# Kernel optimization log

Measured on AMD Instinct MI355X. Metric: run time of the kernel, lower is better.

Reference implementation:

```python
import jax, jax.numpy as jnp
import numpy as np

B, N1, N2, C = 4, 1024, 128, 1152
H, D = 16, 72            # num_heads, head_dim (1152 = 16*72)
HID = 4608               # mlp hidden = 4*1152
ATTN_SCALE = D ** -0.5
RMS_SCALE = C ** 0.5     # quirk: RMSNorm built with dim=1152 though applied over d=72
LN_EPS = 1e-6


def setup_inputs() -> dict:
    key = jax.random.key(0)
    ks = iter(jax.random.split(key, 64))
    n = lambda shape, s=1.0: jax.random.normal(next(ks), shape, jnp.float32) * s
    W = 0.02  # weight init scale
    inp = {
        "x": n((B, N1, C)),
        "c": n((B, N2, C)),
        "global_c": n((B, C)),
        "ada_x_w": n((C, 6 * C), W), "ada_x_b": jnp.zeros((6 * C,)),
        "ada_c_w": n((C, 6 * C), W), "ada_c_b": jnp.zeros((6 * C,)),
        "g1x_g": jnp.ones((C,)), "g1x_b": jnp.zeros((C,)),
        "g2x_g": jnp.ones((C,)), "g2x_b": jnp.zeros((C,)),
        "g1c_g": jnp.ones((C,)), "g1c_b": jnp.zeros((C,)),
        "g2c_g": jnp.ones((C,)), "g2c_b": jnp.zeros((C,)),
        "qkv_x_w": n((C, 3 * C), W), "qkv_x_b": jnp.zeros((3 * C,)),
        "proj_x_w": n((C, C), W), "proj_x_b": jnp.zeros((C,)),
        "qkv_c_w": n((C, 3 * C), W), "qkv_c_b": jnp.zeros((3 * C,)),
        "proj_c_w": n((C, C), W), "proj_c_b": jnp.zeros((C,)),
        "gq_x": jnp.ones((1,)), "gk_x": jnp.ones((1,)),
        "gq_c": jnp.ones((1,)), "gk_c": jnp.ones((1,)),
        "mlp_x_w1": n((C, HID), W), "mlp_x_b1": jnp.zeros((HID,)),
        "mlp_x_w2": n((HID, C), W), "mlp_x_b2": jnp.zeros((C,)),
        "mlp_c_w1": n((C, HID), W), "mlp_c_b1": jnp.zeros((HID,)),
        "mlp_c_w2": n((HID, C), W), "mlp_c_b2": jnp.zeros((C,)),
    }
    return inp


def _ln(t, g, b):
    m = t.mean(-1, keepdims=True)
    v = ((t - m) ** 2).mean(-1, keepdims=True)
    return (t - m) * jax.lax.rsqrt(v + LN_EPS) * g + b


def _modulate(t, shift, scale):  # shift/scale: [B, C]
    return t * (1.0 + scale[:, None, :]) + shift[:, None, :]


def _rms(t, g):  # F.normalize over last dim, then * sqrt(1152) * g
    nrm = jnp.sqrt(jnp.sum(t * t, axis=-1, keepdims=True))
    return t / jnp.maximum(nrm, 1e-12) * (RMS_SCALE * g)


def _heads(t):  # [B, N, H*D] -> [B, H, N, D]
    Bq, Nq, _ = t.shape
    return t.reshape(Bq, Nq, H, D).transpose(0, 2, 1, 3)


def _mmdit_forward(x, c, global_c,
                   ada_x_w, ada_x_b, ada_c_w, ada_c_b,
                   g1x_g, g1x_b, g2x_g, g2x_b, g1c_g, g1c_b, g2c_g, g2c_b,
                   qkv_x_w, qkv_x_b, proj_x_w, proj_x_b,
                   qkv_c_w, qkv_c_b, proj_c_w, proj_c_b,
                   gq_x, gk_x, gq_c, gk_c,
                   mlp_x_w1, mlp_x_b1, mlp_x_w2, mlp_x_b2,
                   mlp_c_w1, mlp_c_b1, mlp_c_w2, mlp_c_b2):
    s = jax.nn.silu(global_c)
    mod_x = jnp.split(s @ ada_x_w + ada_x_b, 6, axis=-1)
    mod_c = jnp.split(s @ ada_c_w + ada_c_b, 6, axis=-1)
    (sh_msa_x, sc_msa_x, gt_msa_x, sh_mlp_x, sc_mlp_x, gt_mlp_x) = mod_x
    (sh_msa_c, sc_msa_c, gt_msa_c, sh_mlp_c, sc_mlp_c, gt_mlp_c) = mod_c

    xin = _modulate(_ln(x, g1x_g, g1x_b), sh_msa_x, sc_msa_x)
    cin = _modulate(_ln(c, g1c_g, g1c_b), sh_msa_c, sc_msa_c)

    qx, kx, vx = jnp.split(xin @ qkv_x_w + qkv_x_b, 3, axis=-1)
    qc, kc, vc = jnp.split(cin @ qkv_c_w + qkv_c_b, 3, axis=-1)
    qx, kx, vx = _heads(qx), _heads(kx), _heads(vx)
    qc, kc, vc = _heads(qc), _heads(kc), _heads(vc)
    qx, kx = _rms(qx, gq_x), _rms(kx, gk_x)
    qc, kc = _rms(qc, gq_c), _rms(kc, gk_c)

    q = jnp.concatenate([qx, qc], axis=2)  # [B,H,N1+N2,D]
    k = jnp.concatenate([kx, kc], axis=2)
    v = jnp.concatenate([vx, vc], axis=2)

    scores = jnp.einsum('bhnd,bhmd->bhnm', q, k) * ATTN_SCALE
    attn = jax.nn.softmax(scores, axis=-1)
    o = jnp.einsum('bhnm,bhmd->bhnd', attn, v)
    o = o.transpose(0, 2, 1, 3).reshape(B, N1 + N2, C)
    ox, oc = o[:, :N1], o[:, N1:]
    attn_x = ox @ proj_x_w + proj_x_b
    attn_c = oc @ proj_c_w + proj_c_b

    x = x + gt_msa_x[:, None, :] * attn_x
    c = c + gt_msa_c[:, None, :] * attn_c

    hx = _modulate(_ln(x, g2x_g, g2x_b), sh_mlp_x, sc_mlp_x)
    hx = jax.nn.gelu(hx @ mlp_x_w1 + mlp_x_b1, approximate=True) @ mlp_x_w2 + mlp_x_b2
    x = x + gt_mlp_x[:, None, :] * hx

    hc = _modulate(_ln(c, g2c_g, g2c_b), sh_mlp_c, sc_mlp_c)
    hc = jax.nn.gelu(hc @ mlp_c_w1 + mlp_c_b1, approximate=True) @ mlp_c_w2 + mlp_c_b2
    c = c + gt_mlp_c[:, None, :] * hc
    return x, c


def reference(x, c, global_c,
              ada_x_w, ada_x_b, ada_c_w, ada_c_b,
              g1x_g, g1x_b, g2x_g, g2x_b, g1c_g, g1c_b, g2c_g, g2c_b,
              qkv_x_w, qkv_x_b, proj_x_w, proj_x_b,
              qkv_c_w, qkv_c_b, proj_c_w, proj_c_b,
              gq_x, gk_x, gq_c, gk_c,
              mlp_x_w1, mlp_x_b1, mlp_x_w2, mlp_x_b2,
              mlp_c_w1, mlp_c_b1, mlp_c_w2, mlp_c_b2):
    return _mmdit_forward(x, c, global_c,
                          ada_x_w, ada_x_b, ada_c_w, ada_c_b,
                          g1x_g, g1x_b, g2x_g, g2x_b, g1c_g, g1c_b, g2c_g, g2c_b,
                          qkv_x_w, qkv_x_b, proj_x_w, proj_x_b,
                          qkv_c_w, qkv_c_b, proj_c_w, proj_c_b,
                          gq_x, gk_x, gq_c, gk_c,
                          mlp_x_w1, mlp_x_b1, mlp_x_w2, mlp_x_b2,
                          mlp_c_w1, mlp_c_b1, mlp_c_w2, mlp_c_b2)
```

## Files before the change

### kernel.cpp

```cpp
#include <hip/hip_runtime.h>

typedef unsigned short u16;
typedef unsigned int u32;
typedef __attribute__((ext_vector_type(8))) short bf16x8;
typedef __attribute__((ext_vector_type(4))) float f32x4;

#define MX_ 4096
#define NT_ 1152
#define C_  1152
#define DP_ 96
#define D_  72
#define H_  16
#define MT_ 4608

static __device__ __forceinline__ float b2f(u16 u){ union{u32 i; float f;} x; x.i=((u32)u)<<16; return x.f; }
static __device__ __forceinline__ u16 f2b(float f){ u32 i=__float_as_uint(f); return (u16)((i + 0x7FFFu + ((i>>16)&1u))>>16); }

static __device__ __forceinline__ void gl_lds16(const u16* g, u16* l){
  __builtin_amdgcn_global_load_lds((const __attribute__((address_space(1))) void*)g,
                                   (__attribute__((address_space(3))) void*)l, 16, 0, 0);
}

#define MFMA16(a,b,c) __builtin_amdgcn_mfma_f32_16x16x32_bf16(a,b,c,0,0,0)

struct TrArgs {
  const float* src[8]; u16* dst[8]; int K[8]; int N[8]; int start[9];
};

__global__ __launch_bounds__(256) void transpose_kernel(TrArgs a){
  int bx = blockIdx.x;
  int mi = 0;
  #pragma unroll
  for (int i = 0; i < 8; ++i) if (bx >= a.start[i+1]) mi = i+1;
  int t = bx - a.start[mi];
  int K = a.K[mi], N = a.N[mi];
  int ntk = K >> 5;
  int tk = t % ntk, tn = t / ntk;
  int k0 = tk*32, n0 = tn*32;
  __shared__ u16 lds[32][33];
  int c = threadIdx.x & 31, r = threadIdx.x >> 5;
  const float* src = a.src[mi];
  u16* dst = a.dst[mi];
  #pragma unroll
  for (int ii = 0; ii < 4; ++ii){
    int row = r + ii*8;
    lds[row][c] = f2b(src[(size_t)(k0+row)*N + n0 + c]);
  }
  __syncthreads();
  #pragma unroll
  for (int ii = 0; ii < 4; ++ii){
    int row = r + ii*8;
    dst[(size_t)(n0+row)*K + k0 + c] = lds[c][row];
  }
}

__global__ __launch_bounds__(256) void ada_kernel(const float* gc, const float* wx, const float* bx,
                                                  const float* wc, const float* bc,
                                                  float* mod_x, float* mod_c){
  __shared__ float s[4][C_];
  __shared__ float part[4][4][64];
  int tid = threadIdx.x;
  for (int i = tid; i < 4*C_; i += 256){
    float v = gc[i];
    s[i / C_][i % C_] = v / (1.f + __expf(-v));
  }
  __syncthreads();
  int jq = tid & 63;
  int kq = tid >> 6;
  int jg = blockIdx.x*64 + jq;
  int which = jg / 6912;
  int j = jg % 6912;
  const float* W = which ? wc : wx;
  float a0=0.f, a1=0.f, a2=0.f, a3=0.f;
  for (int k = kq*288; k < kq*288 + 288; ++k){
    float w = W[(size_t)k*6912 + j];
    a0 += s[0][k]*w; a1 += s[1][k]*w; a2 += s[2][k]*w; a3 += s[3][k]*w;
  }
  part[kq][0][jq]=a0; part[kq][1][jq]=a1; part[kq][2][jq]=a2; part[kq][3][jq]=a3;
  __syncthreads();
  if (kq == 0){
    float bb = (which ? bc : bx)[j];
    float* out = which ? mod_c : mod_x;
    #pragma unroll
    for (int b = 0; b < 4; ++b){
      out[(size_t)b*6912 + j] = part[0][b][jq] + part[1][b][jq] + part[2][b][jq] + part[3][b][jq] + bb;
    }
  }
}

__global__ __launch_bounds__(256) void ln_mod_kernel(
  const float* srcx, const float* srcc, const float* g, const float* bt,
  const float* gcn, const float* btc,
  const float* shx, const float* scx, const float* shc, const float* scc,
  u16* out)
{
  int m = blockIdx.x;
  bool isC = (m >= MX_);
  const float* src = isC ? srcc + (size_t)(m - MX_)*C_ : srcx + (size_t)m*C_;
  int bidx = isC ? ((m - MX_) >> 7) : (m >> 10);
  const float* gg = isC ? gcn : g;
  const float* bb = isC ? btc : bt;
  const float* sh = (isC ? shc : shx) + (size_t)bidx*6912;
  const float* sc = (isC ? scc : scx) + (size_t)bidx*6912;
  int tid = threadIdx.x;
  float lv[8];
  float sum = 0.f, sq = 0.f;
  if (tid < 144){
    float4 v0 = *(const float4*)(src + tid*8);
    float4 v1 = *(const float4*)(src + tid*8 + 4);
    lv[0]=v0.x; lv[1]=v0.y; lv[2]=v0.z; lv[3]=v0.w;
    lv[4]=v1.x; lv[5]=v1.y; lv[6]=v1.z; lv[7]=v1.w;
    #pragma unroll
    for (int j = 0; j < 8; ++j){ sum += lv[j]; sq += lv[j]*lv[j]; }
  }
  #pragma unroll
  for (int off = 1; off < 64; off <<= 1){ sum += __shfl_xor(sum, off); sq += __shfl_xor(sq, off); }
  __shared__ float rs[4], rq[4];
  int wave = tid >> 6, lane = tid & 63;
  if (lane == 0){ rs[wave] = sum; rq[wave] = sq; }
  __syncthreads();
  float S = rs[0]+rs[1]+rs[2]+rs[3];
  float Q = rq[0]+rq[1]+rq[2]+rq[3];
  float mean = S * (1.f/1152.f);
  float var  = Q * (1.f/1152.f) - mean*mean;
  float rstd = rsqrtf(var + 1e-6f);
  if (tid < 144){
    union { uint4 v; u16 s[8]; } o;
    #pragma unroll
    for (int j = 0; j < 8; ++j){
      int n = tid*8 + j;
      float val = (lv[j] - mean)*rstd*gg[n] + bb[n];
      val = val*(1.f + sc[n]) + sh[n];
      o.s[j] = f2b(val);
    }
    *(uint4*)(out + (size_t)m*C_ + tid*8) = o.v;
  }
}

__global__ __launch_bounds__(256) void reduce2_kernel(
  const float* p,
  const float* residx, const float* residc,
  const float* modx, const float* modc,
  const float* biasx, const float* biasc,
  float* outx, float* outc)
{
  for (int i4 = blockIdx.x*256 + threadIdx.x; i4 < MT_*288; i4 += gridDim.x*256){
    int m = i4 / 288, n4 = (i4 % 288)*4;
    bool isC = (m >= MX_);
    int bidx = isC ? ((m - MX_) >> 7) : (m >> 10);
    const float* gate  = (isC ? modc : modx) + (size_t)bidx*6912;
    const float* bias  = isC ? biasc : biasx;
    const float* resid = isC ? residc + (size_t)(m - MX_)*C_ : residx + (size_t)m*C_;
    float* o = isC ? outc + (size_t)(m - MX_)*C_ : outx + (size_t)m*C_;
    float4 a = *(const float4*)(p + (size_t)m*C_ + n4);
    float4 b = *(const float4*)(p + (size_t)(MT_ + m)*C_ + n4);
    float4 r = *(const float4*)(resid + n4);
    float4 ov;
    ov.x = r.x + gate[n4+0]*(a.x + b.x + bias[n4+0]);
    ov.y = r.y + gate[n4+1]*(a.y + b.y + bias[n4+1]);
    ov.z = r.z + gate[n4+2]*(a.z + b.z + bias[n4+2]);
    ov.w = r.w + gate[n4+3]*(a.w + b.w + bias[n4+3]);
    *(float4*)(o + n4) = ov;
  }
}

struct GemmArgs {
  const u16* A; int lda; int rowmap;
  const u16* BTx; const u16* BTc;
  const float* biasx; const float* biasc;
  void* outx; void* outc;
  const float* residx; const float* residc;
  const float* gatex; const float* gatec;
  int N, K, kLen;
};

static __device__ __forceinline__ int amap(int m, int rowmap){
  if (rowmap){
    if (m < MX_) return (m >> 10)*NT_ + (m & 1023);
    int mm = m - MX_;
    return (mm >> 7)*NT_ + 1024 + (mm & 127);
  }
  return m;
}

template<int EPI>
__global__ __launch_bounds__(256, 2) void gemm_kernel(GemmArgs g){
  __shared__ u16 As[128*64];
  __shared__ u16 Bs[128*64];
  int gx = gridDim.x, gy = gridDim.y;
  int nwg = gx*gy;
  int orig = blockIdx.y*gx + blockIdx.x;
  int q = nwg >> 3, r8 = nwg & 7;
  int xcd = orig & 7, wi = orig >> 3;
  int swz = (xcd < r8 ? xcd*(q+1) : r8*(q+1) + (xcd - r8)*q) + wi;
  int n0 = (swz % gx)*128, m0 = (swz / gx)*128;
  int kStart = blockIdx.z * g.kLen;
  bool isC = (m0 >= MX_);
  const u16* BT = isC ? g.BTc : g.BTx;
  int tid = threadIdx.x, wave = tid >> 6, lane = tid & 63;
  int lg = lane >> 4, lr = lane & 15;
  int wm = wave >> 1, wn = wave & 1;
  f32x4 acc[4][4] = {};

  const u16* Aaddr[4]; const u16* Baddr[4];
  #pragma unroll
  for (int i = 0; i < 4; ++i){
    int cb = (wave*4 + i)*64;
    int qq = cb + lane;
    int row = qq >> 3;
    int c16 = (qq & 7) ^ (row & 7);
    Aaddr[i] = g.A + (size_t)amap(m0 + row, g.rowmap)*g.lda + kStart + c16*8;
    Baddr[i] = BT + (size_t)(n0 + row)*g.K + kStart + c16*8;
  }
  for (int k0 = 0; k0 < g.kLen; k0 += 64){
    #pragma unroll
    for (int i = 0; i < 4; ++i){
      int cb = (wave*4 + i)*64;
      gl_lds16(Aaddr[i] + k0, As + cb*8);
      gl_lds16(Baddr[i] + k0, Bs + cb*8);
    }
    __syncthreads();
    #pragma unroll
    for (int kkI = 0; kkI < 2; ++kkI){
      bf16x8 af[4], bfr[4];
      #pragma unroll
      for (int mi = 0; mi < 4; ++mi){
        int row = wm*64 + mi*16 + lr;
        int c16 = (kkI*4 + lg) ^ (row & 7);
        af[mi] = *(const bf16x8*)&As[row*64 + c16*8];
      }
      #pragma unroll
      for (int ni = 0; ni < 4; ++ni){
        int row = wn*64 + ni*16 + lr;
        int c16 = (kkI*4 + lg) ^ (row & 7);
        bfr[ni] = *(const bf16x8*)&Bs[row*64 + c16*8];
      }
      #pragma unroll
      for (int mi = 0; mi < 4; ++mi)
        #pragma unroll
        for (int ni = 0; ni < 4; ++ni)
          acc[mi][ni] = MFMA16(af[mi], bfr[ni], acc[mi][ni]);
    }
    __syncthreads();
  }

  const float* bias  = isC ? g.biasc : g.biasx;
  const float* resid = isC ? g.residc : g.residx;
  void* out = isC ? g.outc : g.outx;
  const float* gate = nullptr;
  if (EPI == 2){
    int bidx = isC ? ((m0 - MX_) >> 7) : (m0 >> 10);
    gate = (isC ? g.gatec : g.gatex) + (size_t)bidx*6912;
  }
  int mbase = isC ? (m0 - MX_) : m0;
  float* pbase = nullptr;
  if (EPI == 3) pbase = (float*)g.outx + (size_t)blockIdx.z*MT_*C_;
  #pragma unroll
  for (int mi = 0; mi < 4; ++mi){
    #pragma unroll
    for (int r = 0; r < 4; ++r){
      #pragma unroll
      for (int ni = 0; ni < 4; ++ni){
        int n = n0 + wn*64 + ni*16 + lr;
        if (EPI == 3){
          size_t prow = (size_t)(m0 + wm*64 + mi*16 + lg*4 + r);
          pbase[prow*(size_t)g.N + n] = acc[mi][ni][r];
        } else {
          size_t orow = (size_t)(mbase + wm*64 + mi*16 + lg*4 + r);
          float v = acc[mi][ni][r] + bias[n];
          if (EPI == 1){
            float u = 0.7978845608028654f*(v + 0.044715f*v*v*v);
            v = 0.5f*v*(1.f + tanhf(u));
          }
          if (EPI == 2){
            v = resid[orow*(size_t)g.N + n] + gate[n]*v;
            ((float*)out)[orow*(size_t)g.N + n] = v;
          } else {
            ((u16*)out)[orow*(size_t)g.N + n] = f2b(v);
          }
        }
      }
    }
  }
}

__global__ __launch_bounds__(256) void rmshead_kernel(
  const u16* qkv, const float* gqx, const float* gkx, const float* gqc, const float* gkc,
  u16* qpad, u16* kpad, u16* vT)
{
  int tt = blockIdx.x, h = blockIdx.y, b = blockIdx.z;
  int t0 = tt*64;
  bool isC = (t0 >= 1024);
  size_t rowbase = isC ? (size_t)(MX_ + b*128 + (t0 - 1024)) : (size_t)(b*1024 + t0);
  __shared__ u16 sq[2][64][72];
  __shared__ u16 sv[64][72];
  __shared__ float nf[2][64];
  int tid = threadIdx.x;
  for (int s = tid; s < 1728; s += 256){
    int which = s / 576, rem = s % 576;
    int t = rem / 9, ch = rem % 9;
    uint4 v = *(const uint4*)(qkv + (rowbase + t)*3456 + which*C_ + h*D_ + ch*8);
    u16* dst = (which < 2) ? &sq[which][t][ch*8] : &sv[t][ch*8];
    *(uint4*)dst = v;
  }
  __syncthreads();
  {
    int row = tid >> 1, half = tid & 1;
    int which = row >> 6, t = row & 63;
    float ss = 0.f;
    for (int d = half*36; d < half*36 + 36; ++d){
      float v = b2f(sq[which][t][d]); ss += v*v;
    }
    ss += __shfl_xor(ss, 1);
    if (half == 0){
      const float* gp = (which == 0) ? (isC ? gqc : gqx) : (isC ? gkc : gkx);
      float f = 33.9411254970f * gp[0] / fmaxf(sqrtf(ss), 1e-12f);
      if (which == 0) f *= 0.11785113019775793f;
      nf[which][t] = f;
    }
  }
  __syncthreads();
  size_t obase = ((size_t)(b*H_ + h)*NT_ + t0) * DP_;
  for (int s = tid; s < 1536; s += 256){
    int which = s / 768, rem = s % 768;
    int t = rem / 12, ch = rem % 12;
    float f = nf[which][t];
    union { uint4 v; u16 e[8]; } o;
    #pragma unroll
    for (int j = 0; j < 8; ++j){
      int d = ch*8 + j;
      o.e[j] = (d < D_) ? f2b(b2f(sq[which][t][d]) * f) : (u16)0;
    }
    *(uint4*)((which == 0 ? qpad : kpad) + obase + (size_t)t*DP_ + ch*8) = o.v;
  }
  size_t vbase = (size_t)(b*H_ + h)*80*NT_;
  for (int s = tid; s < 576; s += 256){
    int d = s / 8, ch = s % 8;
    union { uint4 v; u16 e[8]; } o;
    #pragma unroll
    for (int j = 0; j < 8; ++j) o.e[j] = sv[ch*8 + j][d];
    *(uint4*)(vT + vbase + (size_t)d*NT_ + t0 + ch*8) = o.v;
  }
  for (int s = tid; s < 512; s += 256){
    int d = 72 + (s >> 6), t = s & 63;
    vT[vbase + (size_t)d*NT_ + t0 + t] = (d == 72) ? (u16)0x3F80 : (u16)0;
  }
}

__global__ __launch_bounds__(256) void attn_kernel(
  const u16* qpad, const u16* kpad, const u16* vT, u16* O)
{
  __shared__ u16 Ps[4][32][40];
  int qtb = blockIdx.x, h = blockIdx.y, b = blockIdx.z;
  int bh = b*H_ + h;
  int tid = threadIdx.x, wave = tid >> 6, lane = tid & 63;
  int lg = lane >> 4, lr = lane & 15;
  int q0 = qtb*128 + wave*32;

  const u16* qb = qpad + (size_t)bh*NT_*DP_;
  const u16* kb = kpad + (size_t)bh*NT_*DP_;
  const u16* vb = vT + (size_t)bh*80*NT_;

  bf16x8 qf[2][3];
  #pragma unroll
  for (int qt = 0; qt < 2; ++qt)
    #pragma unroll
    for (int kk = 0; kk < 3; ++kk)
      qf[qt][kk] = *(const bf16x8*)(qb + (size_t)(q0 + qt*16 + lr)*DP_ + kk*32 + lg*8);

  f32x4 acc[5][2] = {};
  float m0 = -1e30f, m1 = -1e30f;

  bf16x8 kfA[2][3], kfB[2][3], vf[5];
  auto LOADK = [&](bf16x8 (&kf)[2][3], int kvt){
    #pragma unroll
    for (int kt = 0; kt < 2; ++kt)
      #pragma unroll
      for (int kk = 0; kk < 3; ++kk)
        kf[kt][kk] = *(const bf16x8*)(kb + (size_t)(kvt*32 + kt*16 + lr)*DP_ + kk*32 + lg*8);
  };
  u16* prow0 = &Ps[wave][lr][0];
  u16* prow1 = &Ps[wave][16 + lr][0];

  auto TILE = [&](bf16x8 (&kf)[2][3], bf16x8 (&kfn)[2][3], int t){
    #pragma unroll
    for (int dc = 0; dc < 5; ++dc)
      vf[dc] = *(const bf16x8*)(vb + (size_t)(dc*16 + lr)*NT_ + t*32 + lg*8);
    if (t + 1 < 36) LOADK(kfn, t + 1);

    f32x4 st[2][2] = {};
    __builtin_amdgcn_s_setprio(1);
    #pragma unroll
    for (int kk = 0; kk < 3; ++kk){
      st[0][0] = MFMA16(kf[0][kk], qf[0][kk], st[0][0]);
      st[0][1] = MFMA16(kf[0][kk], qf[1][kk], st[0][1]);
      st[1][0] = MFMA16(kf[1][kk], qf[0][kk], st[1][0]);
      st[1][1] = MFMA16(kf[1][kk], qf[1][kk], st[1][1]);
    }
    __builtin_amdgcn_s_setprio(0);

    float pm0 = fmaxf(fmaxf(fmaxf(st[0][0][0], st[0][0][1]), fmaxf(st[0][0][2], st[0][0][3])),
                      fmaxf(fmaxf(st[1][0][0], st[1][0][1]), fmaxf(st[1][0][2], st[1][0][3])));
    float pm1 = fmaxf(fmaxf(fmaxf(st[0][1][0], st[0][1][1]), fmaxf(st[0][1][2], st[0][1][3])),
                      fmaxf(fmaxf(st[1][1][0], st[1][1][1]), fmaxf(st[1][1][2], st[1][1][3])));
    float tt = fmaxf(pm0 - m0, pm1 - m1);
    if (!__all(tt <= 8.f)){
      float r0 = fmaxf(pm0, __shfl_xor(pm0, 16)); r0 = fmaxf(r0, __shfl_xor(r0, 32));
      float r1 = fmaxf(pm1, __shfl_xor(pm1, 16)); r1 = fmaxf(r1, __shfl_xor(r1, 32));
      float n0 = fmaxf(m0, r0), n1 = fmaxf(m1, r1);
      float f0 = __expf(m0 - n0), f1 = __expf(m1 - n1);
      m0 = n0; m1 = n1;
      #pragma unroll
      for (int dc = 0; dc < 5; ++dc)
        #pragma unroll
        for (int j = 0; j < 4; ++j){ acc[dc][0][j] *= f0; acc[dc][1][j] *= f1; }
    }
    #pragma unroll
    for (int kt = 0; kt < 2; ++kt){
      #pragma unroll
      for (int qt = 0; qt < 2; ++qt){
        float mm = qt ? m1 : m0;
        u32 w0 = (u32)f2b(__expf(st[kt][qt][0] - mm)) | ((u32)f2b(__expf(st[kt][qt][1] - mm)) << 16);
        u32 w1 = (u32)f2b(__expf(st[kt][qt][2] - mm)) | ((u32)f2b(__expf(st[kt][qt][3] - mm)) << 16);
        uint2 pkd; pkd.x = w0; pkd.y = w1;
        *(uint2*)((qt ? prow1 : prow0) + kt*16 + lg*4) = pkd;
      }
    }
    asm volatile("s_waitcnt lgkmcnt(0)" ::: "memory");
    __builtin_amdgcn_sched_barrier(0);
    bf16x8 bp0 = *(const bf16x8*)(prow0 + lg*8);
    bf16x8 bp1 = *(const bf16x8*)(prow1 + lg*8);
    __builtin_amdgcn_s_setprio(1);
    #pragma unroll
    for (int dc = 0; dc < 5; ++dc){
      acc[dc][0] = MFMA16(vf[dc], bp0, acc[dc][0]);
      acc[dc][1] = MFMA16(vf[dc], bp1, acc[dc][1]);
    }
    __builtin_amdgcn_s_setprio(0);
  };

  LOADK(kfA, 0);
  for (int t2 = 0; t2 < 18; ++t2){
    TILE(kfA, kfB, 2*t2);
    TILE(kfB, kfA, 2*t2 + 1);
  }

  float l0 = __shfl(acc[4][0][0], 32 + lr);
  float l1 = __shfl(acc[4][1][0], 32 + lr);
  float rl0 = 1.f / l0, rl1 = 1.f / l1;
  #pragma unroll
  for (int dc = 0; dc < 5; ++dc){
    #pragma unroll
    for (int qt = 0; qt < 2; ++qt){
      if (dc < 4 || lg < 2){
        float rl = qt ? rl1 : rl0;
        union { uint2 v; u16 e[4]; } o;
        #pragma unroll
        for (int j = 0; j < 4; ++j) o.e[j] = f2b(acc[dc][qt][j] * rl);
        int tok = q0 + qt*16 + lr;
        *(uint2*)(O + ((size_t)b*NT_ + tok)*C_ + h*D_ + dc*16 + lg*4) = o.v;
      }
    }
  }
}

extern "C" void kernel_launch(void* const* d_in, const int* in_sizes, int n_in,
                              void* d_out, int out_size, void* d_ws, size_t ws_size,
                              hipStream_t stream)
{
  (void)in_sizes; (void)n_in; (void)out_size; (void)ws_size;
  const float* x        = (const float*)d_in[0];
  const float* c        = (const float*)d_in[1];
  const float* gc       = (const float*)d_in[2];
  const float* ada_x_w  = (const float*)d_in[3];
  const float* ada_x_b  = (const float*)d_in[4];
  const float* ada_c_w  = (const float*)d_in[5];
  const float* ada_c_b  = (const float*)d_in[6];
  const float* g1x_g    = (const float*)d_in[7];
  const float* g1x_b    = (const float*)d_in[8];
  const float* g2x_g    = (const float*)d_in[9];
  const float* g2x_b    = (const float*)d_in[10];
  const float* g1c_g    = (const float*)d_in[11];
  const float* g1c_b    = (const float*)d_in[12];
  const float* g2c_g    = (const float*)d_in[13];
  const float* g2c_b    = (const float*)d_in[14];
  const float* qkv_x_w  = (const float*)d_in[15];
  const float* qkv_x_b  = (const float*)d_in[16];
  const float* proj_x_w = (const float*)d_in[17];
  const float* proj_x_b = (const float*)d_in[18];
  const float* qkv_c_w  = (const float*)d_in[19];
  const float* qkv_c_b  = (const float*)d_in[20];
  const float* proj_c_w = (const float*)d_in[21];
  const float* proj_c_b = (const float*)d_in[22];
  const float* gq_x     = (const float*)d_in[23];
  const float* gk_x     = (const float*)d_in[24];
  const float* gq_c     = (const float*)d_in[25];
  const float* gk_c     = (const float*)d_in[26];
  const float* m_x_w1   = (const float*)d_in[27];
  const float* m_x_b1   = (const float*)d_in[28];
  const float* m_x_w2   = (const float*)d_in[29];
  const float* m_x_b2   = (const float*)d_in[30];
  const float* m_c_w1   = (const float*)d_in[31];
  const float* m_c_b1   = (const float*)d_in[32];
  const float* m_c_w2   = (const float*)d_in[33];
  const float* m_c_b2   = (const float*)d_in[34];
  float* out = (float*)d_out;

  char* ws = (char*)d_ws;
  size_t off = 0;
  auto alloc = [&](size_t bytes)->void*{ void* p = ws + off; off += (bytes + 255) & ~(size_t)255; return p; };
  u16* WTqx  = (u16*)alloc((size_t)3456*1152*2);
  u16* WTqc  = (u16*)alloc((size_t)3456*1152*2);
  u16* WTpx  = (u16*)alloc((size_t)1152*1152*2);
  u16* WTpc  = (u16*)alloc((size_t)1152*1152*2);
  u16* WTm1x = (u16*)alloc((size_t)4608*1152*2);
  u16* WTm2x = (u16*)alloc((size_t)1152*4608*2);
  u16* WTm1c = (u16*)alloc((size_t)4608*1152*2);
  u16* WTm2c = (u16*)alloc((size_t)1152*4608*2);
  float* mod_x = (float*)alloc((size_t)4*6912*4);
  float* mod_c = (float*)alloc((size_t)4*6912*4);
  u16* xin  = (u16*)alloc((size_t)4608*1152*2);
  u16* pool = (u16*)alloc((size_t)4608*4608*2);
  u16* qpad = (u16*)alloc((size_t)64*1152*96*2 + 4096);
  u16* kpad = (u16*)alloc((size_t)64*1152*96*2 + 4096);
  u16* vTb  = (u16*)alloc((size_t)64*80*1152*2 + 4096);
  u16* Obuf = (u16*)alloc((size_t)4*1152*1152*2);
  float* x1c1 = (float*)alloc((size_t)4608*1152*4);
  float* fc2p = (float*)qpad;

  {
    TrArgs ta;
    const float* srcs[8] = {qkv_x_w, qkv_c_w, proj_x_w, proj_c_w, m_x_w1, m_x_w2, m_c_w1, m_c_w2};
    u16* dsts[8]         = {WTqx, WTqc, WTpx, WTpc, WTm1x, WTm2x, WTm1c, WTm2c};
    int Ks[8] = {1152,1152,1152,1152,1152,4608,1152,4608};
    int Ns[8] = {3456,3456,1152,1152,4608,1152,4608,1152};
    int st = 0;
    for (int i = 0; i < 8; ++i){
      ta.src[i] = srcs[i]; ta.dst[i] = dsts[i]; ta.K[i] = Ks[i]; ta.N[i] = Ns[i];
      ta.start[i] = st; st += (Ks[i]/32)*(Ns[i]/32);
    }
    ta.start[8] = st;
    transpose_kernel<<<dim3(st), dim3(256), 0, stream>>>(ta);
  }
  ada_kernel<<<dim3(216), dim3(256), 0, stream>>>(gc, ada_x_w, ada_x_b, ada_c_w, ada_c_b, mod_x, mod_c);
  ln_mod_kernel<<<dim3(4608), dim3(256), 0, stream>>>(
      x, c, g1x_g, g1x_b, g1c_g, g1c_b,
      mod_x + 0, mod_x + 1152, mod_c + 0, mod_c + 1152, xin);
  {
    GemmArgs ga{};
    ga.A = xin; ga.lda = 1152; ga.rowmap = 0;
    ga.BTx = WTqx; ga.BTc = WTqc; ga.biasx = qkv_x_b; ga.biasc = qkv_c_b;
    ga.outx = pool; ga.outc = pool + (size_t)4096*3456;
    ga.N = 3456; ga.K = 1152; ga.kLen = 1152;
    gemm_kernel<0><<<dim3(27,36), dim3(256), 0, stream>>>(ga);
  }
  rmshead_kernel<<<dim3(18,16,4), dim3(256), 0, stream>>>(pool, gq_x, gk_x, gq_c, gk_c, qpad, kpad, vTb);
  attn_kernel<<<dim3(9,16,4), dim3(256), 0, stream>>>(qpad, kpad, vTb, Obuf);
  {
    GemmArgs ga{};
    ga.A = Obuf; ga.lda = 1152; ga.rowmap = 1;
    ga.BTx = WTpx; ga.BTc = WTpc; ga.biasx = proj_x_b; ga.biasc = proj_c_b;
    ga.outx = x1c1; ga.outc = x1c1 + (size_t)4096*1152;
    ga.residx = x; ga.residc = c;
    ga.gatex = mod_x + 2*1152; ga.gatec = mod_c + 2*1152;
    ga.N = 1152; ga.K = 1152; ga.kLen = 1152;
    gemm_kernel<2><<<dim3(9,36), dim3(256), 0, stream>>>(ga);
  }
  ln_mod_kernel<<<dim3(4608), dim3(256), 0, stream>>>(
      x1c1, x1c1 + (size_t)4096*1152, g2x_g, g2x_b, g2c_g, g2c_b,
      mod_x + 3*1152, mod_x + 4*1152, mod_c + 3*1152, mod_c + 4*1152, xin);
  {
    GemmArgs ga{};
    ga.A = xin; ga.lda = 1152; ga.rowmap = 0;
    ga.BTx = WTm1x; ga.BTc = WTm1c; ga.biasx = m_x_b1; ga.biasc = m_c_b1;
    ga.outx = pool; ga.outc = pool + (size_t)4096*4608;
    ga.N = 4608; ga.K = 1152; ga.kLen = 1152;
    gemm_kernel<1><<<dim3(36,36), dim3(256), 0, stream>>>(ga);
  }
  {
    GemmArgs ga{};
    ga.A = pool; ga.lda = 4608; ga.rowmap = 0;
    ga.BTx = WTm2x; ga.BTc = WTm2c;
    ga.outx = fc2p;
    ga.N = 1152; ga.K = 4608; ga.kLen = 2304;
    gemm_kernel<3><<<dim3(9,36,2), dim3(256), 0, stream>>>(ga);
  }
  reduce2_kernel<<<dim3(2048), dim3(256), 0, stream>>>(
      fc2p, x1c1, x1c1 + (size_t)4096*1152,
      mod_x + 5*1152, mod_c + 5*1152, m_x_b2, m_c_b2,
      out, out + (size_t)4096*1152);
}
```

Measured before the change: 454.9 us.

## Halve attention query tile per wave and remap blocks across XCDs

The attention kernel now gives each wave 16 query rows instead of 32, so each block covers 64 queries and the grid grows from 576 to 1152 blocks. The launch becomes a 1D grid whose block index is remapped so consecutive dispatches land on the same (batch, head), which is meant to improve K/V cache locality per XCD. Launch bounds request 4 blocks per CU to raise occupancy. The cost is that each K/V tile is loaded and reused for half as many queries, which doubles K/V traffic and lowers MFMA work per load.

```diff
diff --git a/kernel.cpp b/kernel.cpp
--- a/kernel.cpp
+++ b/kernel.cpp
@@ -347,29 +347,30 @@
   }
 }
 
-__global__ __launch_bounds__(256) void attn_kernel(
+__global__ __launch_bounds__(256, 4) void attn_kernel(
   const u16* qpad, const u16* kpad, const u16* vT, u16* O)
 {
-  __shared__ u16 Ps[4][32][40];
-  int qtb = blockIdx.x, h = blockIdx.y, b = blockIdx.z;
+  __shared__ u16 Ps[4][16][40];
+  int orig = blockIdx.x;
+  int w = (orig & 7)*144 + (orig >> 3);
+  int qtb = w % 18, hb = w / 18;
+  int h = hb & 15, b = hb >> 4;
   int bh = b*H_ + h;
   int tid = threadIdx.x, wave = tid >> 6, lane = tid & 63;
   int lg = lane >> 4, lr = lane & 15;
-  int q0 = qtb*128 + wave*32;
+  int q0 = qtb*64 + wave*16;
 
   const u16* qb = qpad + (size_t)bh*NT_*DP_;
   const u16* kb = kpad + (size_t)bh*NT_*DP_;
   const u16* vb = vT + (size_t)bh*80*NT_;
 
-  bf16x8 qf[2][3];
-  #pragma unroll
-  for (int qt = 0; qt < 2; ++qt)
-    #pragma unroll
-    for (int kk = 0; kk < 3; ++kk)
-      qf[qt][kk] = *(const bf16x8*)(qb + (size_t)(q0 + qt*16 + lr)*DP_ + kk*32 + lg*8);
-
-  f32x4 acc[5][2] = {};
-  float m0 = -1e30f, m1 = -1e30f;
+  bf16x8 qf[3];
+  #pragma unroll
+  for (int kk = 0; kk < 3; ++kk)
+    qf[kk] = *(const bf16x8*)(qb + (size_t)(q0 + lr)*DP_ + kk*32 + lg*8);
+
+  f32x4 acc[5] = {};
+  float m0 = -1e30f;
 
   bf16x8 kfA[2][3], kfB[2][3], vf[5];
   auto LOADK = [&](bf16x8 (&kf)[2][3], int kvt){
@@ -379,8 +380,7 @@
       for (int kk = 0; kk < 3; ++kk)
         kf[kt][kk] = *(const bf16x8*)(kb + (size_t)(kvt*32 + kt*16 + lr)*DP_ + kk*32 + lg*8);
   };
-  u16* prow0 = &Ps[wave][lr][0];
-  u16* prow1 = &Ps[wave][16 + lr][0];
+  u16* prow = &Ps[wave][lr][0];
 
   auto TILE = [&](bf16x8 (&kf)[2][3], bf16x8 (&kfn)[2][3], int t){
     #pragma unroll
@@ -388,54 +388,41 @@
       vf[dc] = *(const bf16x8*)(vb + (size_t)(dc*16 + lr)*NT_ + t*32 + lg*8);
     if (t + 1 < 36) LOADK(kfn, t + 1);
 
-    f32x4 st[2][2] = {};
+    f32x4 st[2] = {};
     __builtin_amdgcn_s_setprio(1);
     #pragma unroll
     for (int kk = 0; kk < 3; ++kk){
-      st[0][0] = MFMA16(kf[0][kk], qf[0][kk], st[0][0]);
-      st[0][1] = MFMA16(kf[0][kk], qf[1][kk], st[0][1]);
-      st[1][0] = MFMA16(kf[1][kk], qf[0][kk], st[1][0]);
-      st[1][1] = MFMA16(kf[1][kk], qf[1][kk], st[1][1]);
+      st[0] = MFMA16(kf[0][kk], qf[kk], st[0]);
+      st[1] = MFMA16(kf[1][kk], qf[kk], st[1]);
     }
     __builtin_amdgcn_s_setprio(0);
 
-    float pm0 = fmaxf(fmaxf(fmaxf(st[0][0][0], st[0][0][1]), fmaxf(st[0][0][2], st[0][0][3])),
-                      fmaxf(fmaxf(st[1][0][0], st[1][0][1]), fmaxf(st[1][0][2], st[1][0][3])));
-    float pm1 = fmaxf(fmaxf(fmaxf(st[0][1][0], st[0][1][1]), fmaxf(st[0][1][2], st[0][1][3])),
-                      fmaxf(fmaxf(st[1][1][0], st[1][1][1]), fmaxf(st[1][1][2], st[1][1][3])));
-    float tt = fmaxf(pm0 - m0, pm1 - m1);
-    if (!__all(tt <= 8.f)){
+    float pm0 = fmaxf(fmaxf(fmaxf(st[0][0], st[0][1]), fmaxf(st[0][2], st[0][3])),
+                      fmaxf(fmaxf(st[1][0], st[1][1]), fmaxf(st[1][2], st[1][3])));
+    if (!__all(pm0 - m0 <= 8.f)){
       float r0 = fmaxf(pm0, __shfl_xor(pm0, 16)); r0 = fmaxf(r0, __shfl_xor(r0, 32));
-      float r1 = fmaxf(pm1, __shfl_xor(pm1, 16)); r1 = fmaxf(r1, __shfl_xor(r1, 32));
-      float n0 = fmaxf(m0, r0), n1 = fmaxf(m1, r1);
-      float f0 = __expf(m0 - n0), f1 = __expf(m1 - n1);
-      m0 = n0; m1 = n1;
+      float n0 = fmaxf(m0, r0);
+      float f0 = __expf(m0 - n0);
+      m0 = n0;
       #pragma unroll
       for (int dc = 0; dc < 5; ++dc)
         #pragma unroll
-        for (int j = 0; j < 4; ++j){ acc[dc][0][j] *= f0; acc[dc][1][j] *= f1; }
+        for (int j = 0; j < 4; ++j) acc[dc][j] *= f0;
     }
     #pragma unroll
     for (int kt = 0; kt < 2; ++kt){
-      #pragma unroll
-      for (int qt = 0; qt < 2; ++qt){
-        float mm = qt ? m1 : m0;
-        u32 w0 = (u32)f2b(__expf(st[kt][qt][0] - mm)) | ((u32)f2b(__expf(st[kt][qt][1] - mm)) << 16);
-        u32 w1 = (u32)f2b(__expf(st[kt][qt][2] - mm)) | ((u32)f2b(__expf(st[kt][qt][3] - mm)) << 16);
-        uint2 pkd; pkd.x = w0; pkd.y = w1;
-        *(uint2*)((qt ? prow1 : prow0) + kt*16 + lg*4) = pkd;
-      }
+      u32 w0 = (u32)f2b(__expf(st[kt][0] - m0)) | ((u32)f2b(__expf(st[kt][1] - m0)) << 16);
+      u32 w1 = (u32)f2b(__expf(st[kt][2] - m0)) | ((u32)f2b(__expf(st[kt][3] - m0)) << 16);
+      uint2 pkd; pkd.x = w0; pkd.y = w1;
+      *(uint2*)(prow + kt*16 + lg*4) = pkd;
     }
     asm volatile("s_waitcnt lgkmcnt(0)" ::: "memory");
     __builtin_amdgcn_sched_barrier(0);
-    bf16x8 bp0 = *(const bf16x8*)(prow0 + lg*8);
-    bf16x8 bp1 = *(const bf16x8*)(prow1 + lg*8);
+    bf16x8 bp = *(const bf16x8*)(prow + lg*8);
     __builtin_amdgcn_s_setprio(1);
     #pragma unroll
-    for (int dc = 0; dc < 5; ++dc){
-      acc[dc][0] = MFMA16(vf[dc], bp0, acc[dc][0]);
-      acc[dc][1] = MFMA16(vf[dc], bp1, acc[dc][1]);
-    }
+    for (int dc = 0; dc < 5; ++dc)
+      acc[dc] = MFMA16(vf[dc], bp, acc[dc]);
     __builtin_amdgcn_s_setprio(0);
   };
 
@@ -445,21 +432,16 @@
     TILE(kfB, kfA, 2*t2 + 1);
   }
 
-  float l0 = __shfl(acc[4][0][0], 32 + lr);
-  float l1 = __shfl(acc[4][1][0], 32 + lr);
-  float rl0 = 1.f / l0, rl1 = 1.f / l1;
+  float l0 = __shfl(acc[4][0], 32 + lr);
+  float rl0 = 1.f / l0;
   #pragma unroll
   for (int dc = 0; dc < 5; ++dc){
-    #pragma unroll
-    for (int qt = 0; qt < 2; ++qt){
-      if (dc < 4 || lg < 2){
-        float rl = qt ? rl1 : rl0;
-        union { uint2 v; u16 e[4]; } o;
-        #pragma unroll
-        for (int j = 0; j < 4; ++j) o.e[j] = f2b(acc[dc][qt][j] * rl);
-        int tok = q0 + qt*16 + lr;
-        *(uint2*)(O + ((size_t)b*NT_ + tok)*C_ + h*D_ + dc*16 + lg*4) = o.v;
-      }
+    if (dc < 4 || lg < 2){
+      union { uint2 v; u16 e[4]; } o;
+      #pragma unroll
+      for (int j = 0; j < 4; ++j) o.e[j] = f2b(acc[dc][j] * rl0);
+      int tok = q0 + lr;
+      *(uint2*)(O + ((size_t)b*NT_ + tok)*C_ + h*D_ + dc*16 + lg*4) = o.v;
     }
   }
 }
@@ -555,7 +537,7 @@
     gemm_kernel<0><<<dim3(27,36), dim3(256), 0, stream>>>(ga);
   }
   rmshead_kernel<<<dim3(18,16,4), dim3(256), 0, stream>>>(pool, gq_x, gk_x, gq_c, gk_c, qpad, kpad, vTb);
-  attn_kernel<<<dim3(9,16,4), dim3(256), 0, stream>>>(qpad, kpad, vTb, Obuf);
+  attn_kernel<<<dim3(1152), dim3(256), 0, stream>>>(qpad, kpad, vTb, Obuf);
   {
     GemmArgs ga{};
     ga.A = Obuf; ga.lda = 1152; ga.rowmap = 1;
```

New measurement: 512.2 us. 1.13x slower.
